# Kernel tuning notes

Hardware: AMD Instinct MI355X
Metric: run time of the kernel (lower is better)

## Reference

```python
import jax, jax.numpy as jnp
import numpy as np

D_MODEL = 1024
NUM_HEADS = 16
D_K = D_MODEL // NUM_HEADS


def setup_inputs() -> dict:
    key = jax.random.key(0)
    ks = jax.random.split(key, 13)
    B, S = 2, 2048
    s = 1.0 / np.sqrt(D_MODEL)
    inp = {
        'q': jax.random.normal(ks[0], (B, S, D_MODEL), jnp.float32),
        'k': jax.random.normal(ks[1], (B, S, D_MODEL), jnp.float32),
        'v': jax.random.normal(ks[2], (B, S, D_MODEL), jnp.float32),
        'mask': jax.random.randint(ks[3], (B, S), 0, 2, jnp.int32),
        'Wq': jax.random.normal(ks[4], (D_MODEL, D_MODEL), jnp.float32) * s,
        'bq': jax.random.normal(ks[5], (D_MODEL,), jnp.float32) * s,
        'Wk': jax.random.normal(ks[6], (D_MODEL, D_MODEL), jnp.float32) * s,
        'bk': jax.random.normal(ks[7], (D_MODEL,), jnp.float32) * s,
        'Wv': jax.random.normal(ks[8], (D_MODEL, D_MODEL), jnp.float32) * s,
        'bv': jax.random.normal(ks[9], (D_MODEL,), jnp.float32) * s,
        'Wo': jax.random.normal(ks[10], (D_MODEL, D_MODEL), jnp.float32) * s,
        'bo': jax.random.normal(ks[11], (D_MODEL,), jnp.float32) * s,
    }
    return inp


def reference(q, k, v, mask, Wq, bq, Wk, bk, Wv, bv, Wo, bo):
    B, S, _ = q.shape

    def split(x):  # [B,S,D] -> [B,H,S,d_k]
        return x.reshape(B, -1, NUM_HEADS, D_K).transpose(0, 2, 1, 3)

    qh = split(q @ Wq.T + bq)
    kh = split(k @ Wk.T + bk)
    vh = split(v @ Wv.T + bv)

    scores = jnp.einsum('bhqd,bhkd->bhqk', qh, kh) / jnp.sqrt(jnp.float32(D_K))
    scores = jnp.where(mask[:, None, None, :] == 0, jnp.float32(-1e9), scores)
    attn = jax.nn.softmax(scores, axis=-1)
    out = jnp.einsum('bhqk,bhkd->bhqd', attn, vh)  # [B,H,S,d_k]
    out = out.transpose(0, 2, 1, 3).reshape(B, S, NUM_HEADS * D_K)
    return out @ Wo.T + bo
```

## Files before the change

kernel.cpp:

```cpp
#include <hip/hip_runtime.h>
#include <cstdint>
#include <cstddef>


using bf16   = __bf16;
using bf16x4 = __attribute__((ext_vector_type(4))) __bf16;
using bf16x8 = __attribute__((ext_vector_type(8))) __bf16;
using f32x4  = __attribute__((ext_vector_type(4))) float;

#define MFMA_BF16(a, b, c) __builtin_amdgcn_mfma_f32_16x16x32_bf16((a), (b), (c), 0, 0, 0)

__device__ __forceinline__ void gload_lds16(const void* g, void* l) {
  __builtin_amdgcn_global_load_lds((__attribute__((address_space(1))) void*)g,
                                   (__attribute__((address_space(3))) void*)l,
                                   16, 0, 0);
}

#define LOG2E 1.4426950408889634f

__global__ __launch_bounds__(256) void prep_kernel(
    const float* __restrict__ q, const float* __restrict__ k, const float* __restrict__ v,
    const int* __restrict__ mask,
    const float* __restrict__ Wq, const float* __restrict__ Wk,
    const float* __restrict__ Wv, const float* __restrict__ Wo,
    bf16* __restrict__ qb, bf16* __restrict__ kb, bf16* __restrict__ vb,
    bf16* __restrict__ Wqb, bf16* __restrict__ Wkb, bf16* __restrict__ Wvb,
    bf16* __restrict__ Wob, float* __restrict__ maskf)
{
  const int NQ = 1048576;
  const int NW = 262144;
  int i = blockIdx.x * 256 + threadIdx.x;
  if (i < 3 * NQ) {
    const float* src; bf16* dst; int j;
    if (i < NQ)        { src = q; dst = qb; j = i; }
    else if (i < 2*NQ) { src = k; dst = kb; j = i - NQ; }
    else               { src = v; dst = vb; j = i - 2*NQ; }
    float4 f = ((const float4*)src)[j];
    ((bf16x4*)dst)[j] = bf16x4{(bf16)f.x, (bf16)f.y, (bf16)f.z, (bf16)f.w};
  } else if (i < 3*NQ + 4*NW) {
    int j = i - 3*NQ;
    const float* src; bf16* dst;
    if (j < NW)        { src = Wq; dst = Wqb; }
    else if (j < 2*NW) { src = Wk; dst = Wkb; j -= NW; }
    else if (j < 3*NW) { src = Wv; dst = Wvb; j -= 2*NW; }
    else               { src = Wo; dst = Wob; j -= 3*NW; }
    float4 f = ((const float4*)src)[j];
    ((bf16x4*)dst)[j] = bf16x4{(bf16)f.x, (bf16)f.y, (bf16)f.z, (bf16)f.w};
  } else if (i < 3*NQ + 4*NW + 1024) {
    int j = i - 3*NQ - 4*NW;
    int4 mi = ((const int4*)mask)[j];
    float4 o;
    o.x = (mi.x == 0) ? -1e9f * LOG2E : 0.0f;
    o.y = (mi.y == 0) ? -1e9f * LOG2E : 0.0f;
    o.z = (mi.z == 0) ? -1e9f * LOG2E : 0.0f;
    o.w = (mi.w == 0) ? -1e9f * LOG2E : 0.0f;
    ((float4*)maskf)[j] = o;
  }
}

__device__ __forceinline__ void gemm128_core(const bf16* __restrict__ A,
                                             const bf16* __restrict__ Bw,
                                             int K, int m0, int n0,
                                             bf16* As, bf16* Bs, f32x4 acc[4][4])
{
  const int tid  = threadIdx.x;
  const int w    = tid >> 6;
  const int lane = tid & 63;
  const int wr = w >> 1, wc = w & 1;
  const int quad = lane >> 4, l16 = lane & 15;
  const int sw = l16 & 7;
  const int srow8 = lane >> 3;
  const int scol  = ((lane & 7) ^ srow8) * 8;

#pragma unroll
  for (int mt = 0; mt < 4; ++mt)
#pragma unroll
    for (int nt = 0; nt < 4; ++nt)
      acc[mt][nt] = f32x4{0.f, 0.f, 0.f, 0.f};

  for (int k0 = 0; k0 < K; k0 += 64) {
#pragma unroll
    for (int c4 = 0; c4 < 4; ++c4) {
      const int c   = w * 4 + c4;
      const int row = c * 8 + srow8;
      gload_lds16(A  + (size_t)(m0 + row) * K + k0 + scol, As + c * 512);
      gload_lds16(Bw + (size_t)(n0 + row) * K + k0 + scol, Bs + c * 512);
    }
    __syncthreads();
#pragma unroll
    for (int kk = 0; kk < 2; ++kk) {
      bf16x8 af[4], bfr[4];
#pragma unroll
      for (int mt = 0; mt < 4; ++mt)
        af[mt] = *(const bf16x8*)(As + (wr*64 + mt*16 + l16) * 64 + ((kk*4 + quad) ^ sw) * 8);
#pragma unroll
      for (int nt = 0; nt < 4; ++nt)
        bfr[nt] = *(const bf16x8*)(Bs + (wc*64 + nt*16 + l16) * 64 + ((kk*4 + quad) ^ sw) * 8);
#pragma unroll
      for (int mt = 0; mt < 4; ++mt)
#pragma unroll
        for (int nt = 0; nt < 4; ++nt)
          acc[mt][nt] = MFMA_BF16(af[mt], bfr[nt], acc[mt][nt]);
    }
    __syncthreads();
  }
}

__global__ __launch_bounds__(256) void proj3_kernel(
    const bf16* __restrict__ Xq, const bf16* __restrict__ Xk, const bf16* __restrict__ Xv,
    const bf16* __restrict__ Wqb, const bf16* __restrict__ Wkb, const bf16* __restrict__ Wvb,
    const float* __restrict__ bq, const float* __restrict__ bk, const float* __restrict__ bv,
    bf16* __restrict__ qh, bf16* __restrict__ kh, bf16* __restrict__ vhT)
{
  __shared__ bf16 As[128 * 64];
  __shared__ bf16 Bs[128 * 64];
  const int z = blockIdx.z;
  const int m0 = blockIdx.x * 128, n0 = blockIdx.y * 128;

  const int tid = threadIdx.x, w = tid >> 6, lane = tid & 63;
  const int wr = w >> 1, wc = w & 1, quad = lane >> 4, l16 = lane & 15;

  f32x4 acc[4][4];

  if (z == 2) {
    gemm128_core(Wvb, Xv, 1024, n0, m0, As, Bs, acc);
#pragma unroll
    for (int mt = 0; mt < 4; ++mt) {
#pragma unroll
      for (int nt = 0; nt < 4; ++nt) {
        const int tok = m0 + wc*64 + nt*16 + l16;
        const int bb = tok >> 11, s = tok & 2047;
#pragma unroll
        for (int r = 0; r < 4; ++r) {
          const int dv = n0 + wr*64 + mt*16 + quad*4 + r;
          const int h = dv >> 6, d = dv & 63;
          vhT[(((size_t)bb*16 + h)*64 + d)*2048 + s] = (bf16)(acc[mt][nt][r] + bv[dv]);
        }
      }
    }
    return;
  }

  const bf16*  X    = (z == 0) ? Xq  : Xk;
  const bf16*  Wb   = (z == 0) ? Wqb : Wkb;
  const float* bias = (z == 0) ? bq  : bk;
  gemm128_core(X, Wb, 1024, m0, n0, As, Bs, acc);

#pragma unroll
  for (int mt = 0; mt < 4; ++mt) {
#pragma unroll
    for (int nt = 0; nt < 4; ++nt) {
      const int n = n0 + wc*64 + nt*16 + l16;
      const int h = n >> 6, d = n & 63;
      const float bn = bias[n];
#pragma unroll
      for (int r = 0; r < 4; ++r) {
        const int m  = m0 + wr*64 + mt*16 + quad*4 + r;
        const int bb = m >> 11, s = m & 2047;
        const float val = acc[mt][nt][r] + bn;
        if (z == 0)
          qh[(((size_t)bb*16 + h)*2048 + s)*64 + d] = (bf16)(val * (0.125f * LOG2E));
        else
          kh[(((size_t)bb*16 + h)*2048 + s)*64 + d] = (bf16)val;
      }
    }
  }
}

#define PSTRIDE 72

__global__ __launch_bounds__(256, 2) void attn_kernel(
    const bf16* __restrict__ qh, const bf16* __restrict__ kh,
    const bf16* __restrict__ vhT, const float* __restrict__ maskf,
    bf16* __restrict__ out)
{
  __shared__ bf16 Ks[2][64 * 64];
  __shared__ bf16 Vs[2][64 * 64];
  __shared__ bf16 Ps[4][2][16 * PSTRIDE];

  const int tid = threadIdx.x, w = tid >> 6, lane = tid & 63;
  const int quad = lane >> 4, l16 = lane & 15;
  const int sw = l16 & 7;
  const int srow8 = lane >> 3;
  const int scol  = ((lane & 7) ^ srow8) * 8;

  const int L  = blockIdx.x;
  const int bh = (L & 7) + ((L >> 7) << 3);
  const int qt = (L >> 3) & 15;
  const int b  = bh >> 4, h = bh & 15;
  const int q0 = qt * 128 + w * 32;

  const bf16* kbase = kh  + (size_t)bh * 2048 * 64;
  const bf16* vbase = vhT + (size_t)bh * 64 * 2048;
  const bf16* qbase = qh  + ((size_t)bh * 2048 + q0) * 64;
  const float* mbase = maskf + (size_t)b * 2048;

  bf16x8 aQ[2][2];
#pragma unroll
  for (int rb = 0; rb < 2; ++rb)
#pragma unroll
    for (int kk = 0; kk < 2; ++kk)
      aQ[rb][kk] = *(const bf16x8*)(qbase + (size_t)(rb*16 + l16)*64 + kk*32 + quad*8);

  const bf16 one = (bf16)1.0f;
  const bf16x8 aOnes = bf16x8{one, one, one, one, one, one, one, one};

  f32x4 Oacc[2][4];
  f32x4 lacc[2];
#pragma unroll
  for (int rb = 0; rb < 2; ++rb) {
    lacc[rb] = f32x4{0.f,0.f,0.f,0.f};
#pragma unroll
    for (int mb = 0; mb < 4; ++mb) Oacc[rb][mb] = f32x4{0.f,0.f,0.f,0.f};
  }

  auto stage = [&](int t, int buf) {
    const int kt0 = t * 64;
#pragma unroll
    for (int c2 = 0; c2 < 2; ++c2) {
      const int c   = w * 2 + c2;
      const int row = c * 8 + srow8;
      gload_lds16(kbase + (size_t)(kt0 + row) * 64 + scol, &Ks[buf][c * 512]);
      gload_lds16(vbase + (size_t)row * 2048 + kt0 + scol, &Vs[buf][c * 512]);
    }
  };

  stage(0, 0);
  float4 mk[4], mkn[4];
#pragma unroll
  for (int mb = 0; mb < 4; ++mb)
    mk[mb] = *(const float4*)(mbase + mb*16 + quad*4);

  for (int t = 0; t < 32; ++t) {
    const int cur = t & 1;
    __syncthreads();

    if (t < 31) {
      stage(t + 1, cur ^ 1);
      const int kt0n = (t + 1) * 64;
#pragma unroll
      for (int mb = 0; mb < 4; ++mb)
        mkn[mb] = *(const float4*)(mbase + kt0n + mb*16 + quad*4);
    }

    bf16x8 fK[8], fV[8];
#pragma unroll
    for (int mb = 0; mb < 4; ++mb)
#pragma unroll
      for (int kk = 0; kk < 2; ++kk) {
        const int off = (mb*16 + l16)*64 + ((kk*4 + quad) ^ sw)*8;
        fK[mb*2+kk] = *(const bf16x8*)(&Ks[cur][off]);
        fV[mb*2+kk] = *(const bf16x8*)(&Vs[cur][off]);
      }

#pragma unroll
    for (int rb = 0; rb < 2; ++rb) {
      bf16* Pw = Ps[w][rb];
      f32x4 sac[4];
#pragma unroll
      for (int mb = 0; mb < 4; ++mb)
        sac[mb] = f32x4{mk[mb].x, mk[mb].y, mk[mb].z, mk[mb].w};
#pragma unroll
      for (int kk = 0; kk < 2; ++kk)
#pragma unroll
        for (int mb = 0; mb < 4; ++mb)
          sac[mb] = MFMA_BF16(fK[mb*2+kk], aQ[rb][kk], sac[mb]);

      float p[4][4];
#pragma unroll
      for (int mb = 0; mb < 4; ++mb)
#pragma unroll
        for (int r = 0; r < 4; ++r)
          p[mb][r] = exp2f(sac[mb][r]);

#pragma unroll
      for (int mb = 0; mb < 4; ++mb) {
        bf16x4 pk = bf16x4{(bf16)p[mb][0], (bf16)p[mb][1], (bf16)p[mb][2], (bf16)p[mb][3]};
        *(bf16x4*)(Pw + l16*PSTRIDE + mb*16 + quad*4) = pk;
      }
#pragma unroll
      for (int kk = 0; kk < 2; ++kk) {
        bf16x8 aP = *(const bf16x8*)(Pw + l16*PSTRIDE + kk*32 + quad*8);
#pragma unroll
        for (int mb = 0; mb < 4; ++mb)
          Oacc[rb][mb] = MFMA_BF16(fV[mb*2+kk], aP, Oacc[rb][mb]);
        lacc[rb] = MFMA_BF16(aOnes, aP, lacc[rb]);
      }
    }

#pragma unroll
    for (int mb = 0; mb < 4; ++mb) mk[mb] = mkn[mb];
  }

#pragma unroll
  for (int rb = 0; rb < 2; ++rb) {
    const float inv = 1.0f / lacc[rb][0];
#pragma unroll
    for (int mb = 0; mb < 4; ++mb) {
      bf16x4 o = bf16x4{(bf16)(Oacc[rb][mb][0]*inv), (bf16)(Oacc[rb][mb][1]*inv),
                        (bf16)(Oacc[rb][mb][2]*inv), (bf16)(Oacc[rb][mb][3]*inv)};
      *(bf16x4*)(out + ((size_t)b*2048 + q0 + rb*16 + l16)*1024 + h*64 + mb*16 + quad*4) = o;
    }
  }
}

__global__ __launch_bounds__(256) void oproj_kernel(
    const bf16* __restrict__ Ain, const bf16* __restrict__ Wob,
    const float* __restrict__ bo, float* __restrict__ out)
{
  __shared__ bf16 As[64 * 64];
  __shared__ bf16 Bs[128 * 64];
  const int m0 = blockIdx.x * 64, n0 = blockIdx.y * 128;

  const int tid = threadIdx.x, w = tid >> 6, lane = tid & 63;
  const int quad = lane >> 4, l16 = lane & 15;
  const int sw = l16 & 7;
  const int srow8 = lane >> 3;
  const int scol  = ((lane & 7) ^ srow8) * 8;

  f32x4 acc[4][2];
#pragma unroll
  for (int mt = 0; mt < 4; ++mt)
#pragma unroll
    for (int nt = 0; nt < 2; ++nt)
      acc[mt][nt] = f32x4{0.f, 0.f, 0.f, 0.f};

  for (int k0 = 0; k0 < 1024; k0 += 64) {
#pragma unroll
    for (int c4 = 0; c4 < 6; ++c4) {
      const int c = w * 6 + c4;
      if (c < 8) {
        const int row = c * 8 + srow8;
        gload_lds16(Ain + (size_t)(m0 + row) * 1024 + k0 + scol, As + c * 512);
      } else {
        const int cB = c - 8;
        const int row = cB * 8 + srow8;
        gload_lds16(Wob + (size_t)(n0 + row) * 1024 + k0 + scol, Bs + cB * 512);
      }
    }
    __syncthreads();
#pragma unroll
    for (int kk = 0; kk < 2; ++kk) {
      bf16x8 af[4], bfr[2];
#pragma unroll
      for (int mt = 0; mt < 4; ++mt)
        af[mt] = *(const bf16x8*)(As + (mt*16 + l16) * 64 + ((kk*4 + quad) ^ sw) * 8);
#pragma unroll
      for (int nt = 0; nt < 2; ++nt)
        bfr[nt] = *(const bf16x8*)(Bs + (w*32 + nt*16 + l16) * 64 + ((kk*4 + quad) ^ sw) * 8);
#pragma unroll
      for (int mt = 0; mt < 4; ++mt)
#pragma unroll
        for (int nt = 0; nt < 2; ++nt)
          acc[mt][nt] = MFMA_BF16(af[mt], bfr[nt], acc[mt][nt]);
    }
    __syncthreads();
  }

#pragma unroll
  for (int mt = 0; mt < 4; ++mt) {
#pragma unroll
    for (int nt = 0; nt < 2; ++nt) {
      const int n = n0 + w*32 + nt*16 + l16;
      const float bn = bo[n];
#pragma unroll
      for (int r = 0; r < 4; ++r) {
        const int m = m0 + mt*16 + quad*4 + r;
        out[(size_t)m * 1024 + n] = acc[mt][nt][r] + bn;
      }
    }
  }
}

extern "C" void kernel_launch(void* const* d_in, const int* in_sizes, int n_in,
                              void* d_out, int out_size, void* d_ws, size_t ws_size,
                              hipStream_t stream)
{
  const float* q    = (const float*)d_in[0];
  const float* k    = (const float*)d_in[1];
  const float* v    = (const float*)d_in[2];
  const int*   mask = (const int*)d_in[3];
  const float* Wq   = (const float*)d_in[4];
  const float* bq   = (const float*)d_in[5];
  const float* Wk   = (const float*)d_in[6];
  const float* bk   = (const float*)d_in[7];
  const float* Wv   = (const float*)d_in[8];
  const float* bv   = (const float*)d_in[9];
  const float* Wo   = (const float*)d_in[10];
  const float* bo   = (const float*)d_in[11];

  char* ws = (char*)d_ws;
  bf16*  qb    = (bf16*)(ws);
  bf16*  kb    = (bf16*)(ws + (8ull  << 20));
  bf16*  vb    = (bf16*)(ws + (16ull << 20));
  bf16*  Wqb   = (bf16*)(ws + (24ull << 20));
  bf16*  Wkb   = (bf16*)(ws + (26ull << 20));
  bf16*  Wvb   = (bf16*)(ws + (28ull << 20));
  bf16*  Wob   = (bf16*)(ws + (30ull << 20));
  float* maskf = (float*)(ws + (32ull << 20));
  bf16*  qh    = (bf16*)(ws + (33ull << 20));
  bf16*  kh    = (bf16*)(ws + (41ull << 20));
  bf16*  vhT   = (bf16*)(ws + (49ull << 20));
  bf16*  ao    = (bf16*)(ws);
  float* out   = (float*)d_out;

  prep_kernel<<<16388, 256, 0, stream>>>(q, k, v, mask, Wq, Wk, Wv, Wo,
                                         qb, kb, vb, Wqb, Wkb, Wvb, Wob, maskf);
  proj3_kernel<<<dim3(32, 8, 3), 256, 0, stream>>>(qb, kb, vb, Wqb, Wkb, Wvb,
                                                   bq, bk, bv, qh, kh, vhT);
  attn_kernel<<<512, 256, 0, stream>>>(qh, kh, vhT, maskf, ao);
  oproj_kernel<<<dim3(64, 8), 256, 0, stream>>>(ao, Wob, bo, out);
}
```

Before: 250.2 us.

## Enlarge QKV projection tiles and compute softmax denominator with scalar sums

The QKV projection kernel moves from 128x128 tiles to 256x128 tiles on a flat 384-block grid. Each wave now owns a 64x128 slice with 32 accumulators, which raises data reuse per LDS load but increases register pressure under the two-blocks-per-SM launch bound. In the attention kernel, the ones-vector MFMA that produced the row sum is replaced by scalar accumulation of the exponentials plus cross-lane shuffles at the end. The P scratch buffer is also reduced to a single slice per wave, which shrinks LDS use.

```diff
diff --git a/kernel.cpp b/kernel.cpp
--- a/kernel.cpp
+++ b/kernel.cpp
@@ -58,110 +58,106 @@
   }
 }
 
-__device__ __forceinline__ void gemm128_core(const bf16* __restrict__ A,
-                                             const bf16* __restrict__ Bw,
-                                             int K, int m0, int n0,
-                                             bf16* As, bf16* Bs, f32x4 acc[4][4])
-{
-  const int tid  = threadIdx.x;
-  const int w    = tid >> 6;
-  const int lane = tid & 63;
-  const int wr = w >> 1, wc = w & 1;
-  const int quad = lane >> 4, l16 = lane & 15;
-  const int sw = l16 & 7;
-  const int srow8 = lane >> 3;
-  const int scol  = ((lane & 7) ^ srow8) * 8;
-
-#pragma unroll
-  for (int mt = 0; mt < 4; ++mt)
-#pragma unroll
-    for (int nt = 0; nt < 4; ++nt)
-      acc[mt][nt] = f32x4{0.f, 0.f, 0.f, 0.f};
-
-  for (int k0 = 0; k0 < K; k0 += 64) {
-#pragma unroll
-    for (int c4 = 0; c4 < 4; ++c4) {
-      const int c   = w * 4 + c4;
-      const int row = c * 8 + srow8;
-      gload_lds16(A  + (size_t)(m0 + row) * K + k0 + scol, As + c * 512);
-      gload_lds16(Bw + (size_t)(n0 + row) * K + k0 + scol, Bs + c * 512);
-    }
-    __syncthreads();
-#pragma unroll
-    for (int kk = 0; kk < 2; ++kk) {
-      bf16x8 af[4], bfr[4];
-#pragma unroll
-      for (int mt = 0; mt < 4; ++mt)
-        af[mt] = *(const bf16x8*)(As + (wr*64 + mt*16 + l16) * 64 + ((kk*4 + quad) ^ sw) * 8);
-#pragma unroll
-      for (int nt = 0; nt < 4; ++nt)
-        bfr[nt] = *(const bf16x8*)(Bs + (wc*64 + nt*16 + l16) * 64 + ((kk*4 + quad) ^ sw) * 8);
-#pragma unroll
-      for (int mt = 0; mt < 4; ++mt)
-#pragma unroll
-        for (int nt = 0; nt < 4; ++nt)
-          acc[mt][nt] = MFMA_BF16(af[mt], bfr[nt], acc[mt][nt]);
-    }
-    __syncthreads();
-  }
-}
-
-__global__ __launch_bounds__(256) void proj3_kernel(
+__global__ __launch_bounds__(256, 2) void proj3_kernel(
     const bf16* __restrict__ Xq, const bf16* __restrict__ Xk, const bf16* __restrict__ Xv,
     const bf16* __restrict__ Wqb, const bf16* __restrict__ Wkb, const bf16* __restrict__ Wvb,
     const float* __restrict__ bq, const float* __restrict__ bk, const float* __restrict__ bv,
     bf16* __restrict__ qh, bf16* __restrict__ kh, bf16* __restrict__ vhT)
 {
-  __shared__ bf16 As[128 * 64];
+  __shared__ bf16 As[256 * 64];
   __shared__ bf16 Bs[128 * 64];
-  const int z = blockIdx.z;
-  const int m0 = blockIdx.x * 128, n0 = blockIdx.y * 128;
+
+  const int bid = blockIdx.x;
+  const int z   = bid >> 7;
+  const int r_  = bid & 127;
 
   const int tid = threadIdx.x, w = tid >> 6, lane = tid & 63;
-  const int wr = w >> 1, wc = w & 1, quad = lane >> 4, l16 = lane & 15;
-
-  f32x4 acc[4][4];
+  const int quad = lane >> 4, l16 = lane & 15;
+  const int sw = l16 & 7;
+  const int srow8 = lane >> 3;
+  const int scol  = ((lane & 7) ^ srow8) * 8;
+
+  const bf16* Aptr; const bf16* Bptr;
+  int m0, n0;
+  if (z == 2) { Aptr = Wvb; Bptr = Xv; m0 = (r_ >> 5) * 256; n0 = (r_ & 31) * 128; }
+  else        { Aptr = (z == 0) ? Xq : Xk; Bptr = (z == 0) ? Wqb : Wkb;
+                m0 = (r_ >> 3) * 256; n0 = (r_ & 7) * 128; }
+
+  f32x4 acc[4][8];
+#pragma unroll
+  for (int mt = 0; mt < 4; ++mt)
+#pragma unroll
+    for (int nt = 0; nt < 8; ++nt)
+      acc[mt][nt] = f32x4{0.f, 0.f, 0.f, 0.f};
+
+  for (int k0 = 0; k0 < 1024; k0 += 64) {
+#pragma unroll
+    for (int c12 = 0; c12 < 12; ++c12) {
+      const int c = w * 12 + c12;
+      if (c < 32) {
+        const int row = c * 8 + srow8;
+        gload_lds16(Aptr + (size_t)(m0 + row) * 1024 + k0 + scol, As + c * 512);
+      } else {
+        const int cB = c - 32;
+        const int row = cB * 8 + srow8;
+        gload_lds16(Bptr + (size_t)(n0 + row) * 1024 + k0 + scol, Bs + cB * 512);
+      }
+    }
+    __syncthreads();
+#pragma unroll
+    for (int kk = 0; kk < 2; ++kk) {
+      bf16x8 af[4], bf[8];
+#pragma unroll
+      for (int mt = 0; mt < 4; ++mt)
+        af[mt] = *(const bf16x8*)(As + (w*64 + mt*16 + l16) * 64 + ((kk*4 + quad) ^ sw) * 8);
+#pragma unroll
+      for (int nt = 0; nt < 8; ++nt)
+        bf[nt] = *(const bf16x8*)(Bs + (nt*16 + l16) * 64 + ((kk*4 + quad) ^ sw) * 8);
+#pragma unroll
+      for (int mt = 0; mt < 4; ++mt)
+#pragma unroll
+        for (int nt = 0; nt < 8; ++nt)
+          acc[mt][nt] = MFMA_BF16(af[mt], bf[nt], acc[mt][nt]);
+    }
+    __syncthreads();
+  }
 
   if (z == 2) {
-    gemm128_core(Wvb, Xv, 1024, n0, m0, As, Bs, acc);
 #pragma unroll
     for (int mt = 0; mt < 4; ++mt) {
-#pragma unroll
-      for (int nt = 0; nt < 4; ++nt) {
-        const int tok = m0 + wc*64 + nt*16 + l16;
+      const int dvb = m0 + w*64 + mt*16 + quad*4;
+      const float4 bv4 = *(const float4*)(bv + dvb);
+#pragma unroll
+      for (int nt = 0; nt < 8; ++nt) {
+        const int tok = n0 + nt*16 + l16;
         const int bb = tok >> 11, s = tok & 2047;
 #pragma unroll
         for (int r = 0; r < 4; ++r) {
-          const int dv = n0 + wr*64 + mt*16 + quad*4 + r;
+          const int dv = dvb + r;
           const int h = dv >> 6, d = dv & 63;
-          vhT[(((size_t)bb*16 + h)*64 + d)*2048 + s] = (bf16)(acc[mt][nt][r] + bv[dv]);
+          vhT[(((size_t)bb*16 + h)*64 + d)*2048 + s] = (bf16)(acc[mt][nt][r] + (&bv4.x)[r]);
         }
       }
     }
-    return;
-  }
-
-  const bf16*  X    = (z == 0) ? Xq  : Xk;
-  const bf16*  Wb   = (z == 0) ? Wqb : Wkb;
-  const float* bias = (z == 0) ? bq  : bk;
-  gemm128_core(X, Wb, 1024, m0, n0, As, Bs, acc);
-
-#pragma unroll
-  for (int mt = 0; mt < 4; ++mt) {
-#pragma unroll
-    for (int nt = 0; nt < 4; ++nt) {
-      const int n = n0 + wc*64 + nt*16 + l16;
-      const int h = n >> 6, d = n & 63;
-      const float bn = bias[n];
-#pragma unroll
-      for (int r = 0; r < 4; ++r) {
-        const int m  = m0 + wr*64 + mt*16 + quad*4 + r;
-        const int bb = m >> 11, s = m & 2047;
-        const float val = acc[mt][nt][r] + bn;
-        if (z == 0)
-          qh[(((size_t)bb*16 + h)*2048 + s)*64 + d] = (bf16)(val * (0.125f * LOG2E));
-        else
-          kh[(((size_t)bb*16 + h)*2048 + s)*64 + d] = (bf16)val;
+  } else {
+    const float* bias = (z == 0) ? bq : bk;
+#pragma unroll
+    for (int mt = 0; mt < 4; ++mt) {
+#pragma unroll
+      for (int nt = 0; nt < 8; ++nt) {
+        const int n = n0 + nt*16 + l16;
+        const int h = n >> 6, d = n & 63;
+        const float bn = bias[n];
+#pragma unroll
+        for (int r = 0; r < 4; ++r) {
+          const int m  = m0 + w*64 + mt*16 + quad*4 + r;
+          const int bb = m >> 11, s = m & 2047;
+          const float val = acc[mt][nt][r] + bn;
+          if (z == 0)
+            qh[(((size_t)bb*16 + h)*2048 + s)*64 + d] = (bf16)(val * (0.125f * LOG2E));
+          else
+            kh[(((size_t)bb*16 + h)*2048 + s)*64 + d] = (bf16)val;
+        }
       }
     }
   }
@@ -176,7 +172,7 @@
 {
   __shared__ bf16 Ks[2][64 * 64];
   __shared__ bf16 Vs[2][64 * 64];
-  __shared__ bf16 Ps[4][2][16 * PSTRIDE];
+  __shared__ bf16 Ps[4][16 * PSTRIDE];
 
   const int tid = threadIdx.x, w = tid >> 6, lane = tid & 63;
   const int quad = lane >> 4, l16 = lane & 15;
@@ -194,6 +190,7 @@
   const bf16* vbase = vhT + (size_t)bh * 64 * 2048;
   const bf16* qbase = qh  + ((size_t)bh * 2048 + q0) * 64;
   const float* mbase = maskf + (size_t)b * 2048;
+  bf16* Pw = Ps[w];
 
   bf16x8 aQ[2][2];
 #pragma unroll
@@ -202,17 +199,12 @@
     for (int kk = 0; kk < 2; ++kk)
       aQ[rb][kk] = *(const bf16x8*)(qbase + (size_t)(rb*16 + l16)*64 + kk*32 + quad*8);
 
-  const bf16 one = (bf16)1.0f;
-  const bf16x8 aOnes = bf16x8{one, one, one, one, one, one, one, one};
-
   f32x4 Oacc[2][4];
-  f32x4 lacc[2];
-#pragma unroll
-  for (int rb = 0; rb < 2; ++rb) {
-    lacc[rb] = f32x4{0.f,0.f,0.f,0.f};
+  float lsum[2] = {0.f, 0.f};
+#pragma unroll
+  for (int rb = 0; rb < 2; ++rb)
 #pragma unroll
     for (int mb = 0; mb < 4; ++mb) Oacc[rb][mb] = f32x4{0.f,0.f,0.f,0.f};
-  }
 
   auto stage = [&](int t, int buf) {
     const int kt0 = t * 64;
@@ -255,7 +247,6 @@
 
 #pragma unroll
     for (int rb = 0; rb < 2; ++rb) {
-      bf16* Pw = Ps[w][rb];
       f32x4 sac[4];
 #pragma unroll
       for (int mb = 0; mb < 4; ++mb)
@@ -270,8 +261,10 @@
 #pragma unroll
       for (int mb = 0; mb < 4; ++mb)
 #pragma unroll
-        for (int r = 0; r < 4; ++r)
+        for (int r = 0; r < 4; ++r) {
           p[mb][r] = exp2f(sac[mb][r]);
+          lsum[rb] += p[mb][r];
+        }
 
 #pragma unroll
       for (int mb = 0; mb < 4; ++mb) {
@@ -284,7 +277,6 @@
 #pragma unroll
         for (int mb = 0; mb < 4; ++mb)
           Oacc[rb][mb] = MFMA_BF16(fV[mb*2+kk], aP, Oacc[rb][mb]);
-        lacc[rb] = MFMA_BF16(aOnes, aP, lacc[rb]);
       }
     }
 
@@ -294,7 +286,10 @@
 
 #pragma unroll
   for (int rb = 0; rb < 2; ++rb) {
-    const float inv = 1.0f / lacc[rb][0];
+    float l_ = lsum[rb];
+    l_ += __shfl_xor(l_, 16);
+    l_ += __shfl_xor(l_, 32);
+    const float inv = 1.0f / l_;
 #pragma unroll
     for (int mb = 0; mb < 4; ++mb) {
       bf16x4 o = bf16x4{(bf16)(Oacc[rb][mb][0]*inv), (bf16)(Oacc[rb][mb][1]*inv),
@@ -406,8 +401,8 @@
 
   prep_kernel<<<16388, 256, 0, stream>>>(q, k, v, mask, Wq, Wk, Wv, Wo,
                                          qb, kb, vb, Wqb, Wkb, Wvb, Wob, maskf);
-  proj3_kernel<<<dim3(32, 8, 3), 256, 0, stream>>>(qb, kb, vb, Wqb, Wkb, Wvb,
-                                                   bq, bk, bv, qh, kh, vhT);
+  proj3_kernel<<<384, 256, 0, stream>>>(qb, kb, vb, Wqb, Wkb, Wvb,
+                                        bq, bk, bv, qh, kh, vhT);
   attn_kernel<<<512, 256, 0, stream>>>(qh, kh, vhT, maskf, ao);
   oproj_kernel<<<dim3(64, 8), 256, 0, stream>>>(ao, Wob, bo, out);
 }
```

New measurement: 238.0 us. 1.05x faster.
